# Performance work log

Measured on AMD Instinct MI355X. Metric: run time of the kernel, lower is better.

Reference implementation:

```python
import jax, jax.numpy as jnp
import numpy as np


def _normalize(x, axis=-1, eps=1e-12):
    n = jnp.linalg.norm(x, axis=axis, keepdims=True)
    return x / jnp.maximum(n, eps)


def _mlp(x, w1, b1, w2, b2):
    return jnp.maximum(x @ w1 + b1, 0.0) @ w2 + b2


def _quat_mul(a, b):
    # openfold (w, x, y, z) convention, Hamilton product
    aw, ax, ay, az = a[..., 0], a[..., 1], a[..., 2], a[..., 3]
    bw, bx, by, bz = b[..., 0], b[..., 1], b[..., 2], b[..., 3]
    return jnp.stack([
        aw * bw - ax * bx - ay * by - az * bz,
        aw * bx + ax * bw + ay * bz - az * by,
        aw * by - ax * bz + ay * bw + az * bx,
        aw * bz + ax * by - ay * bx + az * bw], axis=-1)


def _quat_rotate(q, v):
    # rotate vector v by unit quaternion q
    w = q[..., :1]
    u = q[..., 1:]
    t = 2.0 * jnp.cross(u, v)
    return v + w * t + jnp.cross(u, t)


def _conj(q):
    return q * jnp.asarray([1.0, -1.0, -1.0, -1.0], dtype=q.dtype)


def setup_inputs() -> dict:
    B, N, P, H, E, M = 2, 384, 128, 64, 32, 64
    key = jax.random.key(0)
    ks = iter(jax.random.split(key, 64))

    def nrm(shape):
        return jax.random.normal(next(ks), shape, dtype=jnp.float32)

    inp = {
        "frames_q": _normalize(nrm((B, N, 4))),
        "frames_x": nrm((B, N, 3)),
        "torsions": nrm((B, N, 7, 2)),
        "h": nrm((B, N, H)),
        "e": nrm((B, N, N, E)),
        "node_mask": jnp.ones((B, N), dtype=bool),
        "pocket_h": nrm((B, P, H)),
        "pocket_e": nrm((B, N, P, E)),
        "pocket_q": _normalize(nrm((B, P, 4))),
        "pocket_x": nrm((B, P, 3)),
        "pocket_mask": jnp.ones((B, P), dtype=bool),
    }
    # 2-layer MLPs with transition_size = 64
    for name, (fin, fout) in {"msg": (2 * H + E + 9, M), "feat": (H + M, H),
                              "tr": (M, 3), "qu": (M, 4), "to": (M, 14)}.items():
        inp[f"{name}_w1"] = nrm((fin, 64)) / np.sqrt(fin)
        inp[f"{name}_b1"] = nrm((64,)) * 0.01
        inp[f"{name}_w2"] = nrm((64, fout)) / np.sqrt(64)
        inp[f"{name}_b2"] = nrm((fout,)) * 0.01
    return inp


def reference(frames_q, frames_x, torsions, h, e, node_mask, pocket_h, pocket_e,
              pocket_q, pocket_x, pocket_mask,
              msg_w1, msg_b1, msg_w2, msg_b2,
              feat_w1, feat_b1, feat_w2, feat_b2,
              tr_w1, tr_b1, tr_w2, tr_b2,
              qu_w1, qu_b1, qu_w2, qu_b2,
              to_w1, to_b1, to_w2, to_b2):
    B, N, Hd = h.shape
    P = pocket_h.shape[-2]

    q_all = jnp.concatenate([frames_q, pocket_q], axis=-2)  # [B, N+P, 4]
    x_all = jnp.concatenate([frames_x, pocket_x], axis=-2)  # [B, N+P, 3]

    eye = jnp.eye(N, dtype=bool)
    mm = jnp.concatenate([
        node_mask[:, :, None] & node_mask[:, None, :] & ~eye,
        node_mask[:, :, None] & pocket_mask[:, None, :]], axis=-1)  # [B, N, N+P]

    vec = frames_x[:, :, None, :] - x_all[:, None, :, :]  # [B, N, N+P, 3]
    d2 = jnp.sum(vec * vec, axis=-1)                       # [B, N, N+P]
    qdot = jnp.abs(jnp.sum(frames_q[:, :, None, :] * q_all[:, None, :, :], axis=-1))

    # global -> local frame of node j applied to node i: R_j^T (x_i - t_j)
    qc = _conj(q_all)[:, None, :, :]                       # [B, 1, N+P, 4]
    local_x = _quat_rotate(qc, vec)                        # [B, N, N+P, 3]
    local_q = _quat_mul(qc, jnp.broadcast_to(frames_q[:, :, None, :], (B, N, N + P, 4)))

    feat = jnp.concatenate([
        jnp.broadcast_to(h[:, :, None, :], (B, N, N + P, Hd)),
        jnp.broadcast_to(jnp.concatenate([h, pocket_h], axis=-2)[:, None, :, :], (B, N, N + P, Hd)),
        jnp.concatenate([e, pocket_e], axis=-2),
        local_x, local_q, d2[..., None], qdot[..., None]], axis=-1)

    m = _mlp(feat, msg_w1, msg_b1, msg_w2, msg_b2) * mm[..., None]  # [B, N, N+P, M]
    msum = jnp.sum(m, axis=-2)                                      # [B, N, M]

    o = _mlp(jnp.concatenate([h, msum], axis=-1), feat_w1, feat_b1, feat_w2, feat_b2)

    dx = _mlp(m, tr_w1, tr_b1, tr_w2, tr_b2) * mm[..., None]        # [B, N, N+P, 3]

    ident = jnp.asarray([1.0, 0.0, 0.0, 0.0], dtype=frames_q.dtype)
    dq = _mlp(msum, qu_w1, qu_b1, qu_w2, qu_b2)
    dq = _normalize(jnp.where(node_mask[..., None], dq, ident))
    upd_q = _quat_mul(frames_q, dq)
    upd_q = _normalize(jnp.where(node_mask[..., None], upd_q, ident))

    qn_all = _normalize(q_all)
    gdx = jnp.sum(_quat_rotate(qn_all[:, None, :, :], dx), axis=-2)  # [B, N, 3]
    n_nb = (node_mask.sum(-1) + pocket_mask.sum(-1) - 1).astype(frames_x.dtype)
    upd_x = frames_x + gdx / n_nb[:, None, None]

    upd_torsions = _normalize(_mlp(msum, to_w1, to_b1, to_w2, to_b2).reshape(torsions.shape))

    return upd_q, upd_x, upd_torsions, o
```

## Files before the change

kernel.cpp:

```cpp
#include <hip/hip_runtime.h>
#include <math.h>

#define BB 2
#define NN 384
#define PP 128
#define HH 64
#define EE 32
#define NP 512
#define K1S 136
#define K2S 72

#define X_OFF (BB*NN*4)
#define T_OFF (X_OFF + BB*NN*3)
#define O_OFF (T_OFF + BB*NN*14)

using bf16x8 = __attribute__((ext_vector_type(8))) __bf16;
using f32x4  = __attribute__((ext_vector_type(4))) float;

__device__ __forceinline__ f32x4 MFMA(bf16x8 a, bf16x8 b, f32x4 c) {
  return __builtin_amdgcn_mfma_f32_16x16x32_bf16(a, b, c, 0, 0, 0);
}
__device__ __forceinline__ bf16x8 LDF(const __bf16* base, int off) {
  return *(const bf16x8*)(base + off);
}
__device__ __forceinline__ bf16x8 pack8(f32x4 lo, f32x4 hi) {
  bf16x8 r;
  r[0]=(__bf16)lo[0]; r[1]=(__bf16)lo[1]; r[2]=(__bf16)lo[2]; r[3]=(__bf16)lo[3];
  r[4]=(__bf16)hi[0]; r[5]=(__bf16)hi[1]; r[6]=(__bf16)hi[2]; r[7]=(__bf16)hi[3];
  return r;
}
__device__ __forceinline__ bf16x8 pack8v(float4 lo, float4 hi) {
  bf16x8 r;
  r[0]=(__bf16)lo.x; r[1]=(__bf16)lo.y; r[2]=(__bf16)lo.z; r[3]=(__bf16)lo.w;
  r[4]=(__bf16)hi.x; r[5]=(__bf16)hi.y; r[6]=(__bf16)hi.z; r[7]=(__bf16)hi.w;
  return r;
}
__device__ __forceinline__ int rowpos(int n) {
  const int t = (n>>5)*2 + ((n>>2)&1);
  const int q = ((n>>3)&3)*4 + (n&3);
  return t*16 + q;
}

__global__ __launch_bounds__(512, 2) void egnn_edge_swapped(
    const float* __restrict__ frames_q, const float* __restrict__ frames_x,
    const float* __restrict__ h, const float* __restrict__ e,
    const int* __restrict__ node_mask,
    const float* __restrict__ pocket_h, const float* __restrict__ pe,
    const float* __restrict__ pocket_q, const float* __restrict__ pocket_x,
    const int* __restrict__ pocket_mask,
    const float* __restrict__ w1, const float* __restrict__ b1,
    const float* __restrict__ w2, const float* __restrict__ b2,
    const float* __restrict__ tw1, const float* __restrict__ tb1,
    const float* __restrict__ tw2, const float* __restrict__ tb2,
    float* __restrict__ msum_ws, float* __restrict__ gdx_ws)
{
  __shared__ __align__(16) __bf16 s_w1p[64*K1S];
  __shared__ __align__(16) __bf16 s_w2p[64*K2S];
  __shared__ __align__(16) __bf16 s_tw1p[64*K2S];
  __shared__ __align__(16) __bf16 s_tw2p[16*K2S];
  __shared__ __align__(16) __bf16 s_geo[NP*16 + 8];
  __shared__ __align__(16) float s_qn[NP*4];
  __shared__ float s_maskf[NP];
  __shared__ float s_b2[64], s_tb1[64], s_tb2[4];
  __shared__ float s_msum[64], s_gdx[3];

  const int tid = threadIdx.x;
  const int b = blockIdx.x / NN, i = blockIdx.x % NN;

  for (int idx = tid; idx < 64*128; idx += 512) {
    const int n = idx & 63, k = idx >> 6;
    float v = 0.f;
    if      (k < 64)  v = w1[(64 + k)*64 + n];
    else if (k < 96)  v = w1[(128 + (k-64))*64 + n];
    else if (k < 105) v = w1[(160 + (k-96))*64 + n];
    s_w1p[rowpos(n)*K1S + k] = (__bf16)v;
  }
  for (int idx = tid; idx < 64*64; idx += 512) {
    const int n = idx & 63, k = idx >> 6;
    s_w2p[rowpos(n)*K2S + k]  = (__bf16)w2[k*64 + n];
    s_tw1p[rowpos(n)*K2S + k] = (__bf16)tw1[k*64 + n];
  }
  for (int idx = tid; idx < 16*64; idx += 512) {
    const int row = idx >> 6, k = idx & 63;
    s_tw2p[row*K2S + k] = (__bf16)((row < 3) ? tw2[k*3 + row] : 0.f);
  }
  if (tid < 64) { s_b2[tid] = b2[tid]; s_tb1[tid] = tb1[tid]; s_msum[tid] = 0.f; }
  if (tid < 8)  s_geo[NP*16 + tid] = (__bf16)0.f;
  if (tid < 3)  { s_tb2[tid] = tb2[tid]; s_gdx[tid] = 0.f; }
  __syncthreads();

  if (tid < 64) {
    const float* hi = &h[(b*NN + i)*HH];
    float a = b1[tid];
#pragma unroll 8
    for (int c = 0; c < 64; ++c) a = fmaf(hi[c], w1[c*64 + tid], a);
    s_w1p[rowpos(tid)*K1S + 105] = (__bf16)a;
  }

  {
    const int j = tid;
    const int maski = node_mask[b*NN + i];
    const float qi0 = frames_q[(b*NN+i)*4+0], qi1 = frames_q[(b*NN+i)*4+1],
                qi2 = frames_q[(b*NN+i)*4+2], qi3 = frames_q[(b*NN+i)*4+3];
    const float xi0 = frames_x[(b*NN+i)*3+0], xi1 = frames_x[(b*NN+i)*3+1],
                xi2 = frames_x[(b*NN+i)*3+2];
    float qj0,qj1,qj2,qj3, xj0,xj1,xj2; int mj;
    if (j < NN) {
      const float4 q4 = *(const float4*)&frames_q[(b*NN+j)*4];
      qj0=q4.x; qj1=q4.y; qj2=q4.z; qj3=q4.w;
      xj0=frames_x[(b*NN+j)*3+0]; xj1=frames_x[(b*NN+j)*3+1]; xj2=frames_x[(b*NN+j)*3+2];
      mj = (node_mask[b*NN+j] != 0) && (j != i);
    } else {
      const int jp = j - NN;
      const float4 q4 = *(const float4*)&pocket_q[(b*PP+jp)*4];
      qj0=q4.x; qj1=q4.y; qj2=q4.z; qj3=q4.w;
      xj0=pocket_x[(b*PP+jp)*3+0]; xj1=pocket_x[(b*PP+jp)*3+1]; xj2=pocket_x[(b*PP+jp)*3+2];
      mj = (pocket_mask[b*PP+jp] != 0);
    }
    const float v0 = xi0 - xj0, v1 = xi1 - xj1, v2 = xi2 - xj2;
    const float d2 = v0*v0 + v1*v1 + v2*v2;
    const float qdot = fabsf(qi0*qj0 + qi1*qj1 + qi2*qj2 + qi3*qj3);
    const float cw = qj0, cx = -qj1, cy = -qj2, cz = -qj3;
    const float t0 = 2.f*(cy*v2 - cz*v1);
    const float t1 = 2.f*(cz*v0 - cx*v2);
    const float t2 = 2.f*(cx*v1 - cy*v0);
    const float lx0 = v0 + cw*t0 + (cy*t2 - cz*t1);
    const float lx1 = v1 + cw*t1 + (cz*t0 - cx*t2);
    const float lx2 = v2 + cw*t2 + (cx*t1 - cy*t0);
    const float lq0 = cw*qi0 - cx*qi1 - cy*qi2 - cz*qi3;
    const float lq1 = cw*qi1 + cx*qi0 + cy*qi3 - cz*qi2;
    const float lq2 = cw*qi2 - cx*qi3 + cy*qi0 + cz*qi1;
    const float lq3 = cw*qi3 + cx*qi2 - cy*qi1 + cz*qi0;
    __bf16* g = &s_geo[j*16];
    g[0]=(__bf16)lx0; g[1]=(__bf16)lx1; g[2]=(__bf16)lx2; g[3]=(__bf16)lq0;
    g[4]=(__bf16)lq1; g[5]=(__bf16)lq2; g[6]=(__bf16)lq3; g[7]=(__bf16)d2;
    g[8]=(__bf16)qdot; g[9]=(__bf16)1.f;
    g[10]=(__bf16)0.f; g[11]=(__bf16)0.f; g[12]=(__bf16)0.f;
    g[13]=(__bf16)0.f; g[14]=(__bf16)0.f; g[15]=(__bf16)0.f;
    s_maskf[j] = (maski && mj) ? 1.f : 0.f;
    const float inv = 1.f / fmaxf(sqrtf(qj0*qj0 + qj1*qj1 + qj2*qj2 + qj3*qj3), 1e-12f);
    float4* qn = (float4*)&s_qn[j*4];
    *qn = make_float4(qj0*inv, qj1*inv, qj2*inv, qj3*inv);
  }
  __syncthreads();

  const int wv = tid >> 6, lane = tid & 63;
  const int l15 = lane & 15, lg = lane >> 4;

  bf16x8 tw2f[2];
  tw2f[0] = *(const bf16x8*)&s_tw2p[l15*K2S +  0 + lg*8];
  tw2f[1] = *(const bf16x8*)&s_tw2p[l15*K2S + 32 + lg*8];

  float b2r[16], tb1r[16];
#pragma unroll
  for (int t2 = 0; t2 < 4; ++t2)
#pragma unroll
    for (int r = 0; r < 4; ++r) {
      const int n2 = (t2>>1)*32 + lg*8 + (t2&1)*4 + r;
      b2r[t2*4 + r]  = s_b2[n2];
      tb1r[t2*4 + r] = s_tb1[n2];
    }
  const float tb2r0 = s_tb2[0], tb2r1 = s_tb2[1], tb2r2 = s_tb2[2];

  float msacc[16];
#pragma unroll
  for (int v = 0; v < 16; ++v) msacc[v] = 0.f;
  float gx0 = 0.f, gx1 = 0.f, gx2 = 0.f;

  const int o1base = l15*K1S + lg*8;
  const int o2base = l15*K2S + lg*8;

#pragma unroll 2
  for (int s = 0; s < 4; ++s) {
    int o1 = o1base; asm volatile("" : "+v"(o1));
    int o2 = o2base; asm volatile("" : "+v"(o2));

    const int jbase = wv*64 + s*16;
    const int j = jbase + l15;
    const bool isn = (jbase < NN);
    const float *hj, *ej;
    if (isn) {
      hj = &h[(b*NN + j)*HH];
      ej = &e[((b*NN + i)*NN + j)*EE];
    } else {
      const int jp = j - NN;
      hj = &pocket_h[(b*PP + jp)*HH];
      ej = &pe[((b*NN + i)*PP + jp)*EE];
    }
    const float mask_f = s_maskf[j];

    const float4 h0 = *(const float4*)&hj[lg*8];
    const float4 h1 = *(const float4*)&hj[lg*8 + 4];
    const float4 h2 = *(const float4*)&hj[32 + lg*8];
    const float4 h3 = *(const float4*)&hj[32 + lg*8 + 4];
    const float4 e0 = *(const float4*)&ej[lg*8];
    const float4 e1 = *(const float4*)&ej[lg*8 + 4];

    const bf16x8 bf0 = pack8v(h0, h1);
    const bf16x8 bf1 = pack8v(h2, h3);
    const bf16x8 bf2 = pack8v(e0, e1);
    const bf16x8 bf3 = *(const bf16x8*)&s_geo[(lg < 2) ? (j*16 + lg*8) : NP*16];

    const f32x4 zero4 = {0.f, 0.f, 0.f, 0.f};
    f32x4 a0 = MFMA(LDF(s_w1p, o1 + 0*16*K1S +  0), bf0, zero4);
    a0 = MFMA(LDF(s_w1p, o1 + 0*16*K1S + 32), bf1, a0);
    a0 = MFMA(LDF(s_w1p, o1 + 0*16*K1S + 64), bf2, a0);
    a0 = MFMA(LDF(s_w1p, o1 + 0*16*K1S + 96), bf3, a0);
    f32x4 a1 = MFMA(LDF(s_w1p, o1 + 1*16*K1S +  0), bf0, zero4);
    a1 = MFMA(LDF(s_w1p, o1 + 1*16*K1S + 32), bf1, a1);
    a1 = MFMA(LDF(s_w1p, o1 + 1*16*K1S + 64), bf2, a1);
    a1 = MFMA(LDF(s_w1p, o1 + 1*16*K1S + 96), bf3, a1);
#pragma unroll
    for (int r = 0; r < 4; ++r) { a0[r] = fmaxf(a0[r], 0.f); a1[r] = fmaxf(a1[r], 0.f); }
    const bf16x8 hb0 = pack8(a0, a1);
    f32x4 a2 = MFMA(LDF(s_w1p, o1 + 2*16*K1S +  0), bf0, zero4);
    a2 = MFMA(LDF(s_w1p, o1 + 2*16*K1S + 32), bf1, a2);
    a2 = MFMA(LDF(s_w1p, o1 + 2*16*K1S + 64), bf2, a2);
    a2 = MFMA(LDF(s_w1p, o1 + 2*16*K1S + 96), bf3, a2);
    f32x4 a3 = MFMA(LDF(s_w1p, o1 + 3*16*K1S +  0), bf0, zero4);
    a3 = MFMA(LDF(s_w1p, o1 + 3*16*K1S + 32), bf1, a3);
    a3 = MFMA(LDF(s_w1p, o1 + 3*16*K1S + 64), bf2, a3);
    a3 = MFMA(LDF(s_w1p, o1 + 3*16*K1S + 96), bf3, a3);
#pragma unroll
    for (int r = 0; r < 4; ++r) { a2[r] = fmaxf(a2[r], 0.f); a3[r] = fmaxf(a3[r], 0.f); }
    const bf16x8 hb1 = pack8(a2, a3);

    f32x4 c0 = MFMA(LDF(s_w2p, o2 + 0*16*K2S +  0), hb0, zero4);
    c0 = MFMA(LDF(s_w2p, o2 + 0*16*K2S + 32), hb1, c0);
    f32x4 c1 = MFMA(LDF(s_w2p, o2 + 1*16*K2S +  0), hb0, zero4);
    c1 = MFMA(LDF(s_w2p, o2 + 1*16*K2S + 32), hb1, c1);
#pragma unroll
    for (int r = 0; r < 4; ++r) {
      c0[r] = (c0[r] + b2r[0*4+r]) * mask_f;  msacc[0*4+r] += c0[r];
      c1[r] = (c1[r] + b2r[1*4+r]) * mask_f;  msacc[1*4+r] += c1[r];
    }
    const bf16x8 mb0 = pack8(c0, c1);
    f32x4 c2 = MFMA(LDF(s_w2p, o2 + 2*16*K2S +  0), hb0, zero4);
    c2 = MFMA(LDF(s_w2p, o2 + 2*16*K2S + 32), hb1, c2);
    f32x4 c3 = MFMA(LDF(s_w2p, o2 + 3*16*K2S +  0), hb0, zero4);
    c3 = MFMA(LDF(s_w2p, o2 + 3*16*K2S + 32), hb1, c3);
#pragma unroll
    for (int r = 0; r < 4; ++r) {
      c2[r] = (c2[r] + b2r[2*4+r]) * mask_f;  msacc[2*4+r] += c2[r];
      c3[r] = (c3[r] + b2r[3*4+r]) * mask_f;  msacc[3*4+r] += c3[r];
    }
    const bf16x8 mb1 = pack8(c2, c3);

    f32x4 d0 = MFMA(LDF(s_tw1p, o2 + 0*16*K2S +  0), mb0, zero4);
    d0 = MFMA(LDF(s_tw1p, o2 + 0*16*K2S + 32), mb1, d0);
    f32x4 d1 = MFMA(LDF(s_tw1p, o2 + 1*16*K2S +  0), mb0, zero4);
    d1 = MFMA(LDF(s_tw1p, o2 + 1*16*K2S + 32), mb1, d1);
#pragma unroll
    for (int r = 0; r < 4; ++r) {
      d0[r] = fmaxf(d0[r] + tb1r[0*4+r], 0.f);
      d1[r] = fmaxf(d1[r] + tb1r[1*4+r], 0.f);
    }
    const bf16x8 thb0 = pack8(d0, d1);
    f32x4 d2f = MFMA(LDF(s_tw1p, o2 + 2*16*K2S +  0), mb0, zero4);
    d2f = MFMA(LDF(s_tw1p, o2 + 2*16*K2S + 32), mb1, d2f);
    f32x4 d3 = MFMA(LDF(s_tw1p, o2 + 3*16*K2S +  0), mb0, zero4);
    d3 = MFMA(LDF(s_tw1p, o2 + 3*16*K2S + 32), mb1, d3);
#pragma unroll
    for (int r = 0; r < 4; ++r) {
      d2f[r] = fmaxf(d2f[r] + tb1r[2*4+r], 0.f);
      d3[r]  = fmaxf(d3[r]  + tb1r[3*4+r], 0.f);
    }
    const bf16x8 thb1 = pack8(d2f, d3);

    f32x4 dacc = MFMA(tw2f[0], thb0, zero4);
    dacc = MFMA(tw2f[1], thb1, dacc);

    if (lg == 0) {
      const float dx0 = (dacc[0] + tb2r0) * mask_f;
      const float dx1 = (dacc[1] + tb2r1) * mask_f;
      const float dx2 = (dacc[2] + tb2r2) * mask_f;
      const float4 qn = *(const float4*)&s_qn[j*4];
      const float w = qn.x, ux = qn.y, uy = qn.z, uz = qn.w;
      const float r0 = 2.f*(uy*dx2 - uz*dx1);
      const float r1 = 2.f*(uz*dx0 - ux*dx2);
      const float r2 = 2.f*(ux*dx1 - uy*dx0);
      gx0 += dx0 + w*r0 + (uy*r2 - uz*r1);
      gx1 += dx1 + w*r1 + (uz*r0 - ux*r2);
      gx2 += dx2 + w*r2 + (ux*r1 - uy*r0);
    }
  }

#pragma unroll
  for (int v = 0; v < 16; ++v) {
    float x = msacc[v];
    x += __shfl_xor(x, 1); x += __shfl_xor(x, 2);
    x += __shfl_xor(x, 4); x += __shfl_xor(x, 8);
    if (l15 == 0) {
      const int n2 = (v>>3)*32 + lg*8 + ((v>>2)&1)*4 + (v&3);
      atomicAdd(&s_msum[n2], x);
    }
  }
  {
    float v0 = (lg == 0) ? gx0 : 0.f;
    float v1 = (lg == 0) ? gx1 : 0.f;
    float v2 = (lg == 0) ? gx2 : 0.f;
#pragma unroll
    for (int sft = 1; sft < 64; sft <<= 1) {
      v0 += __shfl_xor(v0, sft); v1 += __shfl_xor(v1, sft); v2 += __shfl_xor(v2, sft);
    }
    if (lane == 0) { atomicAdd(&s_gdx[0], v0); atomicAdd(&s_gdx[1], v1); atomicAdd(&s_gdx[2], v2); }
  }
  __syncthreads();
  if (tid < 64) msum_ws[(b*NN + i)*64 + tid] = s_msum[tid];
  if (tid >= 64 && tid < 67) gdx_ws[(b*NN + i)*3 + (tid - 64)] = s_gdx[tid - 64];
}

__global__ __launch_bounds__(64) void egnn_node_kernel(
    const float* __restrict__ frames_q, const float* __restrict__ frames_x,
    const float* __restrict__ h,
    const int* __restrict__ node_mask, const int* __restrict__ pocket_mask,
    const float* __restrict__ fw1, const float* __restrict__ fb1,
    const float* __restrict__ fw2, const float* __restrict__ fb2,
    const float* __restrict__ qw1, const float* __restrict__ qb1,
    const float* __restrict__ qw2, const float* __restrict__ qb2,
    const float* __restrict__ tow1, const float* __restrict__ tob1,
    const float* __restrict__ tow2, const float* __restrict__ tob2,
    const float* __restrict__ msum_ws, const float* __restrict__ gdx_ws,
    float* __restrict__ out)
{
  const int t  = threadIdx.x;
  const int bi = blockIdx.x;
  const int b = bi / NN, i = bi % NN;
  __shared__ float s_h[64], s_ms[64], s_hid[64], s_tmp[16];

  s_h[t]  = h[(b*NN+i)*HH + t];
  s_ms[t] = msum_ws[(b*NN+i)*64 + t];

  int cnt = 0;
  for (int k = t; k < NN; k += 64) cnt += (node_mask[b*NN+k] != 0);
  for (int k = t; k < PP; k += 64) cnt += (pocket_mask[b*PP+k] != 0);
  cnt += __shfl_xor(cnt,1); cnt += __shfl_xor(cnt,2); cnt += __shfl_xor(cnt,4);
  cnt += __shfl_xor(cnt,8); cnt += __shfl_xor(cnt,16); cnt += __shfl_xor(cnt,32);
  const float n_nb = (float)(cnt - 1);

  __syncthreads();
  float a = fb1[t];
  for (int k = 0; k < 64; ++k) a = fmaf(s_h[k],  fw1[k*64 + t], a);
  for (int k = 0; k < 64; ++k) a = fmaf(s_ms[k], fw1[(64+k)*64 + t], a);
  s_hid[t] = fmaxf(a, 0.f);
  __syncthreads();
  float ov = fb2[t];
  for (int k = 0; k < 64; ++k) ov = fmaf(s_hid[k], fw2[k*64 + t], ov);
  out[O_OFF + (b*NN+i)*64 + t] = ov;

  __syncthreads();
  float aq = qb1[t];
  for (int k = 0; k < 64; ++k) aq = fmaf(s_ms[k], qw1[k*64 + t], aq);
  s_hid[t] = fmaxf(aq, 0.f);
  __syncthreads();
  if (t < 4) {
    float d = qb2[t];
    for (int k = 0; k < 64; ++k) d = fmaf(s_hid[k], qw2[k*4 + t], d);
    s_tmp[t] = d;
  }
  __syncthreads();
  if (t == 0) {
    const int mi = node_mask[b*NN+i];
    float d0,d1,d2,d3;
    if (mi) { d0=s_tmp[0]; d1=s_tmp[1]; d2=s_tmp[2]; d3=s_tmp[3]; }
    else    { d0=1.f; d1=0.f; d2=0.f; d3=0.f; }
    float nrm = fmaxf(sqrtf(d0*d0+d1*d1+d2*d2+d3*d3), 1e-12f);
    d0/=nrm; d1/=nrm; d2/=nrm; d3/=nrm;
    const float q0=frames_q[(b*NN+i)*4+0], q1=frames_q[(b*NN+i)*4+1],
                q2=frames_q[(b*NN+i)*4+2], q3=frames_q[(b*NN+i)*4+3];
    float u0 = q0*d0 - q1*d1 - q2*d2 - q3*d3;
    float u1 = q0*d1 + q1*d0 + q2*d3 - q3*d2;
    float u2 = q0*d2 - q1*d3 + q2*d0 + q3*d1;
    float u3 = q0*d3 + q1*d2 - q2*d1 + q3*d0;
    if (!mi) { u0=1.f; u1=0.f; u2=0.f; u3=0.f; }
    float nrm2 = fmaxf(sqrtf(u0*u0+u1*u1+u2*u2+u3*u3), 1e-12f);
    out[(b*NN+i)*4+0]=u0/nrm2; out[(b*NN+i)*4+1]=u1/nrm2;
    out[(b*NN+i)*4+2]=u2/nrm2; out[(b*NN+i)*4+3]=u3/nrm2;
  }
  if (t < 3) {
    out[X_OFF + (b*NN+i)*3 + t] = frames_x[(b*NN+i)*3+t] + gdx_ws[(b*NN+i)*3+t] / n_nb;
  }

  __syncthreads();
  float at = tob1[t];
  for (int k = 0; k < 64; ++k) at = fmaf(s_ms[k], tow1[k*64 + t], at);
  s_hid[t] = fmaxf(at, 0.f);
  __syncthreads();
  if (t < 14) {
    float v = tob2[t];
    for (int k = 0; k < 64; ++k) v = fmaf(s_hid[k], tow2[k*14 + t], v);
    s_tmp[t] = v;
  }
  __syncthreads();
  if (t < 14) {
    const int p = t & ~1;
    const float a0 = s_tmp[p], a1 = s_tmp[p+1];
    const float nrm = fmaxf(sqrtf(a0*a0 + a1*a1), 1e-12f);
    out[T_OFF + (b*NN+i)*14 + t] = s_tmp[t] / nrm;
  }
}

extern "C" void kernel_launch(void* const* d_in, const int* in_sizes, int n_in,
                              void* d_out, int out_size, void* d_ws, size_t ws_size,
                              hipStream_t stream) {
  const float* frames_q    = (const float*)d_in[0];
  const float* frames_x    = (const float*)d_in[1];
  const float* h           = (const float*)d_in[3];
  const float* e           = (const float*)d_in[4];
  const int*   node_mask   = (const int*)d_in[5];
  const float* pocket_h    = (const float*)d_in[6];
  const float* pocket_e    = (const float*)d_in[7];
  const float* pocket_q    = (const float*)d_in[8];
  const float* pocket_x    = (const float*)d_in[9];
  const int*   pocket_mask = (const int*)d_in[10];
  const float* msg_w1 = (const float*)d_in[11];
  const float* msg_b1 = (const float*)d_in[12];
  const float* msg_w2 = (const float*)d_in[13];
  const float* msg_b2 = (const float*)d_in[14];
  const float* feat_w1 = (const float*)d_in[15];
  const float* feat_b1 = (const float*)d_in[16];
  const float* feat_w2 = (const float*)d_in[17];
  const float* feat_b2 = (const float*)d_in[18];
  const float* tr_w1 = (const float*)d_in[19];
  const float* tr_b1 = (const float*)d_in[20];
  const float* tr_w2 = (const float*)d_in[21];
  const float* tr_b2 = (const float*)d_in[22];
  const float* qu_w1 = (const float*)d_in[23];
  const float* qu_b1 = (const float*)d_in[24];
  const float* qu_w2 = (const float*)d_in[25];
  const float* qu_b2 = (const float*)d_in[26];
  const float* to_w1 = (const float*)d_in[27];
  const float* to_b1 = (const float*)d_in[28];
  const float* to_w2 = (const float*)d_in[29];
  const float* to_b2 = (const float*)d_in[30];

  float* out = (float*)d_out;
  float* msum_ws = (float*)d_ws;
  float* gdx_ws  = msum_ws + BB*NN*64;

  egnn_edge_swapped<<<dim3(BB*NN), dim3(512), 0, stream>>>(
      frames_q, frames_x, h, e, node_mask,
      pocket_h, pocket_e, pocket_q, pocket_x, pocket_mask,
      msg_w1, msg_b1, msg_w2, msg_b2,
      tr_w1, tr_b1, tr_w2, tr_b2,
      msum_ws, gdx_ws);

  egnn_node_kernel<<<dim3(BB*NN), dim3(64), 0, stream>>>(
      frames_q, frames_x, h, node_mask, pocket_mask,
      feat_w1, feat_b1, feat_w2, feat_b2,
      qu_w1, qu_b1, qu_w2, qu_b2,
      to_w1, to_b1, to_w2, to_b2,
      msum_ws, gdx_ws, out);
}
```

Measured before the change: 63.83 us.

## Shrink LDS footprint and raise occupancy to three blocks per CU

```diff
diff --git a/kernel.cpp b/kernel.cpp
--- a/kernel.cpp
+++ b/kernel.cpp
@@ -41,7 +41,7 @@
   return t*16 + q;
 }
 
-__global__ __launch_bounds__(512, 2) void egnn_edge_swapped(
+__global__ __launch_bounds__(512, 3) void egnn_edge_swapped(
     const float* __restrict__ frames_q, const float* __restrict__ frames_x,
     const float* __restrict__ h, const float* __restrict__ e,
     const int* __restrict__ node_mask,
@@ -58,8 +58,8 @@
   __shared__ __align__(16) __bf16 s_w2p[64*K2S];
   __shared__ __align__(16) __bf16 s_tw1p[64*K2S];
   __shared__ __align__(16) __bf16 s_tw2p[16*K2S];
-  __shared__ __align__(16) __bf16 s_geo[NP*16 + 8];
-  __shared__ __align__(16) float s_qn[NP*4];
+  __shared__ __align__(16) __bf16 s_geoA[NP*8];
+  __shared__ float s_qd[NP];
   __shared__ float s_maskf[NP];
   __shared__ float s_b2[64], s_tb1[64], s_tb2[4];
   __shared__ float s_msum[64], s_gdx[3];
@@ -73,7 +73,7 @@
     if      (k < 64)  v = w1[(64 + k)*64 + n];
     else if (k < 96)  v = w1[(128 + (k-64))*64 + n];
     else if (k < 105) v = w1[(160 + (k-96))*64 + n];
-    s_w1p[rowpos(n)*K1S + k] = (__bf16)v;
+    if (k != 105) s_w1p[rowpos(n)*K1S + k] = (__bf16)v;
   }
   for (int idx = tid; idx < 64*64; idx += 512) {
     const int n = idx & 63, k = idx >> 6;
@@ -85,16 +85,16 @@
     s_tw2p[row*K2S + k] = (__bf16)((row < 3) ? tw2[k*3 + row] : 0.f);
   }
   if (tid < 64) { s_b2[tid] = b2[tid]; s_tb1[tid] = tb1[tid]; s_msum[tid] = 0.f; }
-  if (tid < 8)  s_geo[NP*16 + tid] = (__bf16)0.f;
   if (tid < 3)  { s_tb2[tid] = tb2[tid]; s_gdx[tid] = 0.f; }
-  __syncthreads();
-
-  if (tid < 64) {
+
+  {
+    const int n = tid >> 3, part = tid & 7;
     const float* hi = &h[(b*NN + i)*HH];
-    float a = b1[tid];
-#pragma unroll 8
-    for (int c = 0; c < 64; ++c) a = fmaf(hi[c], w1[c*64 + tid], a);
-    s_w1p[rowpos(tid)*K1S + 105] = (__bf16)a;
+    float a = 0.f;
+#pragma unroll
+    for (int c = 0; c < 8; ++c) a = fmaf(hi[part*8 + c], w1[(part*8 + c)*64 + n], a);
+    a += __shfl_xor(a, 1); a += __shfl_xor(a, 2); a += __shfl_xor(a, 4);
+    if (part == 0) s_w1p[rowpos(n)*K1S + 105] = (__bf16)(a + b1[n]);
   }
 
   {
@@ -131,16 +131,12 @@
     const float lq1 = cw*qi1 + cx*qi0 + cy*qi3 - cz*qi2;
     const float lq2 = cw*qi2 - cx*qi3 + cy*qi0 + cz*qi1;
     const float lq3 = cw*qi3 + cx*qi2 - cy*qi1 + cz*qi0;
-    __bf16* g = &s_geo[j*16];
+    bf16x8 g;
     g[0]=(__bf16)lx0; g[1]=(__bf16)lx1; g[2]=(__bf16)lx2; g[3]=(__bf16)lq0;
     g[4]=(__bf16)lq1; g[5]=(__bf16)lq2; g[6]=(__bf16)lq3; g[7]=(__bf16)d2;
-    g[8]=(__bf16)qdot; g[9]=(__bf16)1.f;
-    g[10]=(__bf16)0.f; g[11]=(__bf16)0.f; g[12]=(__bf16)0.f;
-    g[13]=(__bf16)0.f; g[14]=(__bf16)0.f; g[15]=(__bf16)0.f;
+    *(bf16x8*)&s_geoA[j*8] = g;
+    s_qd[j] = qdot;
     s_maskf[j] = (maski && mj) ? 1.f : 0.f;
-    const float inv = 1.f / fmaxf(sqrtf(qj0*qj0 + qj1*qj1 + qj2*qj2 + qj3*qj3), 1e-12f);
-    float4* qn = (float4*)&s_qn[j*4];
-    *qn = make_float4(qj0*inv, qj1*inv, qj2*inv, qj3*inv);
   }
   __syncthreads();
 
@@ -178,14 +174,16 @@
     const int jbase = wv*64 + s*16;
     const int j = jbase + l15;
     const bool isn = (jbase < NN);
-    const float *hj, *ej;
+    const float *hj, *ej, *qjp;
     if (isn) {
-      hj = &h[(b*NN + j)*HH];
-      ej = &e[((b*NN + i)*NN + j)*EE];
+      hj  = &h[(b*NN + j)*HH];
+      ej  = &e[((b*NN + i)*NN + j)*EE];
+      qjp = &frames_q[(b*NN + j)*4];
     } else {
       const int jp = j - NN;
-      hj = &pocket_h[(b*PP + jp)*HH];
-      ej = &pe[((b*NN + i)*PP + jp)*EE];
+      hj  = &pocket_h[(b*PP + jp)*HH];
+      ej  = &pe[((b*NN + i)*PP + jp)*EE];
+      qjp = &pocket_q[(b*PP + jp)*4];
     }
     const float mask_f = s_maskf[j];
 
@@ -195,11 +193,17 @@
     const float4 h3 = *(const float4*)&hj[32 + lg*8 + 4];
     const float4 e0 = *(const float4*)&ej[lg*8];
     const float4 e1 = *(const float4*)&ej[lg*8 + 4];
+    const float4 qj4 = *(const float4*)qjp;
 
     const bf16x8 bf0 = pack8v(h0, h1);
     const bf16x8 bf1 = pack8v(h2, h3);
     const bf16x8 bf2 = pack8v(e0, e1);
-    const bf16x8 bf3 = *(const bf16x8*)&s_geo[(lg < 2) ? (j*16 + lg*8) : NP*16];
+    const float qd = s_qd[j];
+    const bf16x8 gA = *(const bf16x8*)&s_geoA[j*8];
+    bf16x8 bf3;
+#pragma unroll
+    for (int r8 = 0; r8 < 8; ++r8) bf3[r8] = (lg == 0) ? gA[r8] : (__bf16)0.f;
+    if (lg == 1) { bf3[0] = (__bf16)qd; bf3[1] = (__bf16)1.f; }
 
     const f32x4 zero4 = {0.f, 0.f, 0.f, 0.f};
     f32x4 a0 = MFMA(LDF(s_w1p, o1 + 0*16*K1S +  0), bf0, zero4);
@@ -274,8 +278,8 @@
       const float dx0 = (dacc[0] + tb2r0) * mask_f;
       const float dx1 = (dacc[1] + tb2r1) * mask_f;
       const float dx2 = (dacc[2] + tb2r2) * mask_f;
-      const float4 qn = *(const float4*)&s_qn[j*4];
-      const float w = qn.x, ux = qn.y, uy = qn.z, uz = qn.w;
+      const float inv = 1.f / fmaxf(sqrtf(qj4.x*qj4.x + qj4.y*qj4.y + qj4.z*qj4.z + qj4.w*qj4.w), 1e-12f);
+      const float w = qj4.x*inv, ux = qj4.y*inv, uy = qj4.z*inv, uz = qj4.w*inv;
       const float r0 = 2.f*(uy*dx2 - uz*dx1);
       const float r1 = 2.f*(uz*dx0 - ux*dx2);
       const float r2 = 2.f*(ux*dx1 - uy*dx0);
```

After: 72.25 us. 13.2% more time.

## Prefetch next strip of h/e loads and parallelize per-row h·W1 precompute

Applied to the files above, without the earlier changes.

```diff
diff --git a/kernel.cpp b/kernel.cpp
--- a/kernel.cpp
+++ b/kernel.cpp
@@ -73,7 +73,7 @@
     if      (k < 64)  v = w1[(64 + k)*64 + n];
     else if (k < 96)  v = w1[(128 + (k-64))*64 + n];
     else if (k < 105) v = w1[(160 + (k-96))*64 + n];
-    s_w1p[rowpos(n)*K1S + k] = (__bf16)v;
+    if (k != 105) s_w1p[rowpos(n)*K1S + k] = (__bf16)v;
   }
   for (int idx = tid; idx < 64*64; idx += 512) {
     const int n = idx & 63, k = idx >> 6;
@@ -87,14 +87,15 @@
   if (tid < 64) { s_b2[tid] = b2[tid]; s_tb1[tid] = tb1[tid]; s_msum[tid] = 0.f; }
   if (tid < 8)  s_geo[NP*16 + tid] = (__bf16)0.f;
   if (tid < 3)  { s_tb2[tid] = tb2[tid]; s_gdx[tid] = 0.f; }
-  __syncthreads();
-
-  if (tid < 64) {
+
+  {
+    const int n = tid >> 3, part = tid & 7;
     const float* hi = &h[(b*NN + i)*HH];
-    float a = b1[tid];
-#pragma unroll 8
-    for (int c = 0; c < 64; ++c) a = fmaf(hi[c], w1[c*64 + tid], a);
-    s_w1p[rowpos(tid)*K1S + 105] = (__bf16)a;
+    float a = 0.f;
+#pragma unroll
+    for (int c = 0; c < 8; ++c) a = fmaf(hi[part*8 + c], w1[(part*8 + c)*64 + n], a);
+    a += __shfl_xor(a, 1); a += __shfl_xor(a, 2); a += __shfl_xor(a, 4);
+    if (part == 0) s_w1p[rowpos(n)*K1S + 105] = (__bf16)(a + b1[n]);
   }
 
   {
@@ -170,35 +171,43 @@
   const int o1base = l15*K1S + lg*8;
   const int o2base = l15*K2S + lg*8;
 
-#pragma unroll 2
+#define LOADSTRIP(S, H0_,H1_,H2_,H3_,E0_,E1_) do {                          \
+    const int jbase_ = wv*64 + (S)*16;                                      \
+    const int j_ = jbase_ + l15;                                            \
+    const float *hj_, *ej_;                                                 \
+    if (jbase_ < NN) {                                                      \
+      hj_ = &h[(b*NN + j_)*HH];                                             \
+      ej_ = &e[((b*NN + i)*NN + j_)*EE];                                    \
+    } else {                                                                \
+      const int jp_ = j_ - NN;                                              \
+      hj_ = &pocket_h[(b*PP + jp_)*HH];                                     \
+      ej_ = &pe[((b*NN + i)*PP + jp_)*EE];                                  \
+    }                                                                       \
+    H0_ = *(const float4*)&hj_[lg*8];                                       \
+    H1_ = *(const float4*)&hj_[lg*8 + 4];                                   \
+    H2_ = *(const float4*)&hj_[32 + lg*8];                                  \
+    H3_ = *(const float4*)&hj_[32 + lg*8 + 4];                              \
+    E0_ = *(const float4*)&ej_[lg*8];                                       \
+    E1_ = *(const float4*)&ej_[lg*8 + 4];                                   \
+  } while (0)
+
+  float4 cH0, cH1, cH2, cH3, cE0, cE1;
+  float4 nH0, nH1, nH2, nH3, nE0, nE1;
+  LOADSTRIP(0, cH0, cH1, cH2, cH3, cE0, cE1);
+
+#pragma unroll
   for (int s = 0; s < 4; ++s) {
+    if (s < 3) LOADSTRIP(s+1, nH0, nH1, nH2, nH3, nE0, nE1);
+
     int o1 = o1base; asm volatile("" : "+v"(o1));
     int o2 = o2base; asm volatile("" : "+v"(o2));
 
-    const int jbase = wv*64 + s*16;
-    const int j = jbase + l15;
-    const bool isn = (jbase < NN);
-    const float *hj, *ej;
-    if (isn) {
-      hj = &h[(b*NN + j)*HH];
-      ej = &e[((b*NN + i)*NN + j)*EE];
-    } else {
-      const int jp = j - NN;
-      hj = &pocket_h[(b*PP + jp)*HH];
-      ej = &pe[((b*NN + i)*PP + jp)*EE];
-    }
+    const int j = wv*64 + s*16 + l15;
     const float mask_f = s_maskf[j];
 
-    const float4 h0 = *(const float4*)&hj[lg*8];
-    const float4 h1 = *(const float4*)&hj[lg*8 + 4];
-    const float4 h2 = *(const float4*)&hj[32 + lg*8];
-    const float4 h3 = *(const float4*)&hj[32 + lg*8 + 4];
-    const float4 e0 = *(const float4*)&ej[lg*8];
-    const float4 e1 = *(const float4*)&ej[lg*8 + 4];
-
-    const bf16x8 bf0 = pack8v(h0, h1);
-    const bf16x8 bf1 = pack8v(h2, h3);
-    const bf16x8 bf2 = pack8v(e0, e1);
+    const bf16x8 bf0 = pack8v(cH0, cH1);
+    const bf16x8 bf1 = pack8v(cH2, cH3);
+    const bf16x8 bf2 = pack8v(cE0, cE1);
     const bf16x8 bf3 = *(const bf16x8*)&s_geo[(lg < 2) ? (j*16 + lg*8) : NP*16];
 
     const f32x4 zero4 = {0.f, 0.f, 0.f, 0.f};
@@ -283,7 +292,12 @@
       gx1 += dx1 + w*r1 + (uz*r0 - ux*r2);
       gx2 += dx2 + w*r2 + (ux*r1 - uy*r0);
     }
-  }
+
+    if (s < 3) {
+      cH0 = nH0; cH1 = nH1; cH2 = nH2; cH3 = nH3; cE0 = nE0; cE1 = nE1;
+    }
+  }
+#undef LOADSTRIP
 
 #pragma unroll
   for (int v = 0; v < 16; ++v) {
```

Result: slower. 65.92 us (+3.3%).
